# Performance work log

Measured on AMD Instinct MI355X. Metric: run time of the kernel, lower is better.

Reference implementation:

```python
import jax, jax.numpy as jnp
import numpy as np

# dims
B, S, H = 2, 256, 1024          # batch, global seq, global hidden
BH, NH = 384, 8                  # byte_hidden, num heads
HD = BH // NH                    # head dim = 48
P = 4                            # num_global_proj (seed byte positions)
S_C = 12                         # byte decode steps (= target.shape[2])
L = 4                            # num_byte_decoder_layers
V = 258                          # byte vocab (256 bytes + pad 256 + eos 257)
T = P + S_C
EOS = 257
SCALE = 1.0 / np.sqrt(HD)


def setup_inputs() -> dict:
    key = jax.random.key(0)
    ks = jax.random.split(key, 12)
    w = lambda k, shp: jax.random.normal(k, shp, jnp.float32) * 0.02
    return {
        "x": jax.random.normal(ks[0], (B, S, H), jnp.float32),
        "target": jax.random.randint(ks[1], (B, S, S_C), 0, V),
        "Wproj": w(ks[2], (H, P * BH)),
        "attn_norm": jnp.ones((L, BH), jnp.float32),
        "Wq": w(ks[3], (L, BH, BH)),
        "Wk": w(ks[4], (L, BH, BH)),
        "Wv": w(ks[5], (L, BH, BH)),
        "Wo": w(ks[6], (L, BH, BH)),
        "ffn_norm": jnp.ones((L, BH), jnp.float32),
        "W1": w(ks[7], (L, BH, 4 * BH)),
        "W2": w(ks[8], (L, 4 * BH, BH)),
        "Wlm": w(ks[9], (BH, V)),
    }


def _rms(x, g):
    return x * jax.lax.rsqrt(jnp.mean(x * x, -1, keepdims=True) + 1e-5) * g


def _block(x, kc, vc, pos, an, Wq, Wk, Wv, Wo, fn, W1, W2, causal):
    # x: [N, Lq, BH]; kc/vc: [N, T, NH, HD] KV caches; pos: static write offset
    N, Lq, _ = x.shape
    h = _rms(x, an)
    q = (h @ Wq).reshape(N, Lq, NH, HD)
    k = (h @ Wk).reshape(N, Lq, NH, HD)
    v = (h @ Wv).reshape(N, Lq, NH, HD)
    kc = jax.lax.dynamic_update_slice(kc, k, (0, pos, 0, 0))
    vc = jax.lax.dynamic_update_slice(vc, v, (0, pos, 0, 0))
    nk = pos + Lq
    sc = jnp.einsum('nqhd,nkhd->nhqk', q, kc[:, :nk]) * SCALE
    if causal:
        mask = jnp.arange(nk)[None, :] <= (pos + jnp.arange(Lq))[:, None]
        sc = jnp.where(mask[None, None], sc, jnp.float32(-1e30))
    p = jax.nn.softmax(sc, axis=-1)
    o = jnp.einsum('nhqk,nkhd->nqhd', p, vc[:, :nk]).reshape(N, Lq, BH)
    x = x + o @ Wo
    x = x + jax.nn.gelu(_rms(x, fn) @ W1, approximate=False) @ W2
    return x, kc, vc


def _forward(x, Wproj, attn_norm, Wq, Wk, Wv, Wo, ffn_norm, W1, W2, Wlm):
    N = B * S
    x0 = (x.reshape(N, H) @ Wproj).reshape(N, P, BH)
    x_out = jnp.zeros((N, T, BH), x0.dtype).at[:, :P].set(x0)
    kc = [jnp.zeros((N, T, NH, HD), x0.dtype) for _ in range(L)]
    vc = [jnp.zeros((N, T, NH, HD), x0.dtype) for _ in range(L)]
    finished = jnp.zeros((N,), bool)
    for i in range(S_C):
        if i == 0:
            pos, xi, causal = 0, x_out[:, :P], True          # prefill seed bytes
        else:
            pos, xi, causal = P + i - 1, x_out[:, P + i - 1:P + i], False  # decode 1 token
        for l in range(L):
            xi, kc[l], vc[l] = _block(xi, kc[l], vc[l], pos,
                                      attn_norm[l], Wq[l], Wk[l], Wv[l], Wo[l],
                                      ffn_norm[l], W1[l], W2[l], causal)
        gen = xi[:, -1]                                       # [N, BH]
        unf = ~finished
        # scatter only unfinished streams back (finished stay zero, as in torch)
        x_out = x_out.at[:, P + i].set(jnp.where(unf[:, None], gen, jnp.float32(0.0)))
        finished = finished | (unf & (jnp.argmax(gen, -1) == EOS))
    return x_out.reshape(B, S, T, BH)[:, :, P:, :] @ Wlm      # [B,S,S_C,V]


def reference(x, target, Wproj, attn_norm, Wq, Wk, Wv, Wo, ffn_norm, W1, W2, Wlm):
    del target  # only sets S_c (static here)
    return _forward(x, Wproj, attn_norm, Wq, Wk, Wv, Wo, ffn_norm, W1, W2, Wlm)
```

## Files before the change

kernel.cpp:

```cpp
#include <hip/hip_runtime.h>
#include <hip/hip_bf16.h>


constexpr int H_IN  = 1024;
constexpr int BH    = 384;
constexpr int NH    = 8;
constexpr int HD    = 48;
constexpr int PP    = 4;
constexpr int S_CNT = 12;
constexpr int NL    = 4;
constexpr int NV    = 258;
constexpr int TT    = 16;
constexpr int NSEQ  = 512;
constexpr int EOS_I = 257;
constexpr int NTH   = 768;
constexpr float RSCALE = 0.14433756729740646f;

typedef _Float16 h2 __attribute__((ext_vector_type(2)));
typedef _Float16 h8 __attribute__((ext_vector_type(8)));

union W16 { h8 v8; h2 h[4]; _Float16 e[8]; };

template<int N> struct IC { static constexpr int value = N; };

__device__ __forceinline__ float fdot2(h2 a, h2 b, float c) {
#if __has_builtin(__builtin_amdgcn_fdot2)
  return __builtin_amdgcn_fdot2(a, b, c, false);
#else
  return c + (float)a.x * (float)b.x + (float)a.y * (float)b.y;
#endif
}

__global__ __launch_bounds__(256)
void pack8_kernel(const float* __restrict__ src, const float* __restrict__ g,
                  h8* __restrict__ dst, int C) {
  int c  = blockIdx.x * 256 + threadIdx.x;
  int j8 = blockIdx.y;
  if (c < C) {
    h8 v;
    #pragma unroll
    for (int r = 0; r < 8; r++) {
      int row = 8 * j8 + r;
      float s = g ? g[row] : 1.0f;
      v[r] = (_Float16)(src[(size_t)row * C + c] * s);
    }
    dst[(size_t)j8 * C + c] = v;
  }
}

__global__ __launch_bounds__(NTH)
void decoder_kernel(const float* __restrict__ x,
                    const h8* __restrict__ Wproj8,
                    const h8* __restrict__ Wq8,
                    const h8* __restrict__ Wk8,
                    const h8* __restrict__ Wv8,
                    const h8* __restrict__ Wo8,
                    const h8* __restrict__ W18,
                    const h8* __restrict__ W28,
                    const h8* __restrict__ Wlm8,
                    float* __restrict__ out,
                    _Float16* __restrict__ kbuf,
                    _Float16* __restrict__ vbuf)
{
  __shared__ float xs[2][4][BH];
  __shared__ __align__(16) _Float16 xh[2][4][BH];
  __shared__ __align__(16) _Float16 qh[2][4][BH];
  __shared__ __align__(16) _Float16 oh[2][4][BH];
  __shared__ float sc[2][NH][4][TT];
  __shared__ __align__(16) union Scr {
    float qkvp[3][2][4][BH];
    float wop[2][4][BH];
    struct { __align__(16) _Float16 f1h[2][4][4*BH];
             float w2p[2][4][BH]; } ffn;
    __align__(16) _Float16 xin[2][H_IN];
  } scr;
  __shared__ float redsq[2][4][6];
  __shared__ float redv[12];
  __shared__ int   redi[12];
  __shared__ int   fin[2];

  const int tid = threadIdx.x;
  const int kg  = tid / BH;
  const int col = tid - kg * BH;
  const int sq  = kg;
  const int wid = tid >> 6;
  const int w6  = wid % 6;
  const int seq0 = blockIdx.x * 2;

  if (tid < 2) fin[tid] = 0;

  for (int s = 0; s < 2; s++) {
    const size_t base = (size_t)(seq0 + s) * H_IN;
    for (int j = tid; j < H_IN; j += NTH) scr.xin[s][j] = (_Float16)x[base + j];
  }
  __syncthreads();
  {
    float acc[2][2] = {};
    for (int j8 = 0; j8 < H_IN / 8; j8 += 4) {
      W16 w0[4], w1[4];
      #pragma unroll
      for (int u = 0; u < 4; u++) {
        w0[u].v8 = Wproj8[(size_t)(j8 + u) * (PP * BH) + tid];
        w1[u].v8 = Wproj8[(size_t)(j8 + u) * (PP * BH) + tid + NTH];
      }
      #pragma unroll
      for (int u = 0; u < 4; u++)
        #pragma unroll
        for (int s = 0; s < 2; s++) {
          W16 hv; hv.v8 = *(const h8*)&scr.xin[s][(j8 + u) * 8];
          #pragma unroll
          for (int r = 0; r < 4; r++) {
            acc[s][0] = fdot2(hv.h[r], w0[u].h[r], acc[s][0]);
            acc[s][1] = fdot2(hv.h[r], w1[u].h[r], acc[s][1]);
          }
        }
    }
    const int m0 = tid / BH, cc = tid - m0 * BH;
    #pragma unroll
    for (int s = 0; s < 2; s++) {
      xs[s][m0][cc]     = acc[s][0];  xh[s][m0][cc]     = (_Float16)acc[s][0];
      xs[s][m0 + 2][cc] = acc[s][1];  xh[s][m0 + 2][cc] = (_Float16)acc[s][1];
      float r0 = acc[s][0] * acc[s][0], r1 = acc[s][1] * acc[s][1];
      #pragma unroll
      for (int off = 32; off; off >>= 1) {
        r0 += __shfl_down(r0, off, 64); r1 += __shfl_down(r1, off, 64);
      }
      if ((tid & 63) == 0) { redsq[s][m0][w6] = r0; redsq[s][m0 + 2][w6] = r1; }
    }
  }
  __syncthreads();

  auto layers = [&](auto ntc, int pos, bool causal) {
    constexpr int NT = decltype(ntc)::value;
    const int nk = pos + NT;
    for (int l = 0; l < NL; l++) {
      {
        const size_t wb = ((size_t)l * 48 + kg * 24) * BH + col;
        float aq[2][NT] = {}, ak[2][NT] = {}, av[2][NT] = {};
        for (int j8 = 0; j8 < 24; j8 += 4) {
          W16 wq[4], wk[4], wv[4];
          #pragma unroll
          for (int u = 0; u < 4; u++) {
            wq[u].v8 = Wq8[wb + (size_t)(j8 + u) * BH];
            wk[u].v8 = Wk8[wb + (size_t)(j8 + u) * BH];
            wv[u].v8 = Wv8[wb + (size_t)(j8 + u) * BH];
          }
          #pragma unroll
          for (int u = 0; u < 4; u++)
            #pragma unroll
            for (int s = 0; s < 2; s++)
              #pragma unroll
              for (int tok = 0; tok < NT; tok++) {
                W16 hv; hv.v8 = *(const h8*)&xh[s][tok][(kg * 24 + j8 + u) * 8];
                #pragma unroll
                for (int r = 0; r < 4; r++) {
                  aq[s][tok] = fdot2(hv.h[r], wq[u].h[r], aq[s][tok]);
                  ak[s][tok] = fdot2(hv.h[r], wk[u].h[r], ak[s][tok]);
                  av[s][tok] = fdot2(hv.h[r], wv[u].h[r], av[s][tok]);
                }
              }
        }
        if (kg == 1) {
          #pragma unroll
          for (int s = 0; s < 2; s++)
            #pragma unroll
            for (int tok = 0; tok < NT; tok++) {
              scr.qkvp[0][s][tok][col] = aq[s][tok];
              scr.qkvp[1][s][tok][col] = ak[s][tok];
              scr.qkvp[2][s][tok][col] = av[s][tok];
            }
        }
        __syncthreads();
        if (kg == 0) {
          #pragma unroll
          for (int s = 0; s < 2; s++) {
            const size_t cb = (((size_t)(seq0 + s) * NL + l) * TT + pos) * BH + col;
            #pragma unroll
            for (int tok = 0; tok < NT; tok++) {
              float ss = redsq[s][tok][0] + redsq[s][tok][1] + redsq[s][tok][2] +
                         redsq[s][tok][3] + redsq[s][tok][4] + redsq[s][tok][5];
              float sca = rsqrtf(ss * (1.0f / BH) + 1e-5f);
              qh[s][tok][col] = (_Float16)((aq[s][tok] + scr.qkvp[0][s][tok][col]) * sca * RSCALE);
              kbuf[cb + (size_t)tok * BH] = (_Float16)((ak[s][tok] + scr.qkvp[1][s][tok][col]) * sca);
              vbuf[cb + (size_t)tok * BH] = (_Float16)((av[s][tok] + scr.qkvp[2][s][tok][col]) * sca);
            }
          }
        }
        __syncthreads();
      }
      {
        const int nu = 2 * NH * NT * nk;
        if (tid < nu) {
          int s = tid / (NH * NT * nk), r = tid % (NH * NT * nk);
          int h = r / (NT * nk); int r2 = r % (NT * nk);
          int qi = r2 / nk, j = r2 % nk;
          float d;
          if (causal && j > pos + qi) d = -1e30f;
          else {
            const h8* kp8 = (const h8*)(kbuf + (((size_t)(seq0 + s) * NL + l) * TT + j) * BH + h * HD);
            W16 kk[6];
            #pragma unroll
            for (int c = 0; c < 6; c++) kk[c].v8 = kp8[c];
            d = 0.f;
            #pragma unroll
            for (int c = 0; c < 6; c++)
              #pragma unroll
              for (int e = 0; e < 8; e++)
                d += (float)qh[s][qi][h * HD + c * 8 + e] * (float)kk[c].e[e];
          }
          sc[s][h][qi][j] = d;
        }
      }
      __syncthreads();
      {
        const int nr = 2 * NH * NT;
        if (tid < nr) {
          int s = tid / (NH * NT), r = tid % (NH * NT);
          int h = r / NT, qi = r % NT;
          float m = -3.0e38f;
          for (int j = 0; j < nk; j++) m = fmaxf(m, sc[s][h][qi][j]);
          float den = 0.f;
          for (int j = 0; j < nk; j++) {
            float e = expf(sc[s][h][qi][j] - m);
            sc[s][h][qi][j] = e; den += e;
          }
          float inv = 1.0f / den;
          for (int j = 0; j < nk; j++) sc[s][h][qi][j] *= inv;
        }
      }
      __syncthreads();
      {
        const size_t vb = (((size_t)(seq0 + sq) * NL + l) * TT) * BH + col;
        const int h = col / HD;
        #pragma unroll
        for (int tok = 0; tok < NT; tok++) {
          float acc = 0.f;
          int j = 0;
          for (; j + 4 <= nk; j += 4) {
            float v0 = (float)vbuf[vb + (size_t)(j + 0) * BH];
            float v1 = (float)vbuf[vb + (size_t)(j + 1) * BH];
            float v2 = (float)vbuf[vb + (size_t)(j + 2) * BH];
            float v3 = (float)vbuf[vb + (size_t)(j + 3) * BH];
            acc += sc[sq][h][tok][j] * v0 + sc[sq][h][tok][j+1] * v1 +
                   sc[sq][h][tok][j+2] * v2 + sc[sq][h][tok][j+3] * v3;
          }
          for (; j < nk; j++)
            acc += sc[sq][h][tok][j] * (float)vbuf[vb + (size_t)j * BH];
          oh[sq][tok][col] = (_Float16)acc;
        }
      }
      __syncthreads();
      {
        const size_t wb = ((size_t)l * 48 + kg * 24) * BH + col;
        float ao[2][NT] = {};
        for (int j8 = 0; j8 < 24; j8 += 8) {
          W16 w[8];
          #pragma unroll
          for (int u = 0; u < 8; u++) w[u].v8 = Wo8[wb + (size_t)(j8 + u) * BH];
          #pragma unroll
          for (int u = 0; u < 8; u++)
            #pragma unroll
            for (int s = 0; s < 2; s++)
              #pragma unroll
              for (int tok = 0; tok < NT; tok++) {
                W16 hv; hv.v8 = *(const h8*)&oh[s][tok][(kg * 24 + j8 + u) * 8];
                #pragma unroll
                for (int r = 0; r < 4; r++)
                  ao[s][tok] = fdot2(hv.h[r], w[u].h[r], ao[s][tok]);
              }
        }
        if (kg == 1) {
          #pragma unroll
          for (int s = 0; s < 2; s++)
            #pragma unroll
            for (int tok = 0; tok < NT; tok++) scr.wop[s][tok][col] = ao[s][tok];
        }
        __syncthreads();
        if (kg == 0) {
          #pragma unroll
          for (int s = 0; s < 2; s++)
            #pragma unroll
            for (int tok = 0; tok < NT; tok++) {
              float xn = xs[s][tok][col] + ao[s][tok] + scr.wop[s][tok][col];
              xs[s][tok][col] = xn; xh[s][tok][col] = (_Float16)xn;
              float r = xn * xn;
              #pragma unroll
              for (int off = 32; off; off >>= 1) r += __shfl_down(r, off, 64);
              if ((tid & 63) == 0) redsq[s][tok][wid] = r;
            }
        }
        __syncthreads();
      }
      {
        float a1[2][NT][2] = {};
        for (int j8 = 0; j8 < 48; j8 += 4) {
          W16 w0[4], w1[4];
          #pragma unroll
          for (int u = 0; u < 4; u++) {
            w0[u].v8 = W18[((size_t)(l * 48 + j8 + u)) * (4 * BH) + tid];
            w1[u].v8 = W18[((size_t)(l * 48 + j8 + u)) * (4 * BH) + tid + NTH];
          }
          #pragma unroll
          for (int u = 0; u < 4; u++)
            #pragma unroll
            for (int s = 0; s < 2; s++)
              #pragma unroll
              for (int t = 0; t < NT; t++) {
                W16 hv; hv.v8 = *(const h8*)&xh[s][t][(j8 + u) * 8];
                #pragma unroll
                for (int r = 0; r < 4; r++) {
                  a1[s][t][0] = fdot2(hv.h[r], w0[u].h[r], a1[s][t][0]);
                  a1[s][t][1] = fdot2(hv.h[r], w1[u].h[r], a1[s][t][1]);
                }
              }
        }
        #pragma unroll
        for (int s = 0; s < 2; s++)
          #pragma unroll
          for (int t = 0; t < NT; t++) {
            float ss = redsq[s][t][0] + redsq[s][t][1] + redsq[s][t][2] +
                       redsq[s][t][3] + redsq[s][t][4] + redsq[s][t][5];
            float sca = rsqrtf(ss * (1.0f / BH) + 1e-5f);
            float z0 = a1[s][t][0] * sca, z1 = a1[s][t][1] * sca;
            scr.ffn.f1h[s][t][tid]       = (_Float16)(0.5f * z0 * (1.0f + erff(z0 * 0.7071067811865476f)));
            scr.ffn.f1h[s][t][tid + NTH] = (_Float16)(0.5f * z1 * (1.0f + erff(z1 * 0.7071067811865476f)));
          }
        __syncthreads();
        {
          float a2[2][NT] = {};
          for (int j8 = 0; j8 < 96; j8 += 8) {
            W16 w[8];
            #pragma unroll
            for (int u = 0; u < 8; u++)
              w[u].v8 = W28[((size_t)(l * 192 + kg * 96 + j8 + u)) * BH + col];
            #pragma unroll
            for (int u = 0; u < 8; u++)
              #pragma unroll
              for (int s = 0; s < 2; s++)
                #pragma unroll
                for (int t = 0; t < NT; t++) {
                  W16 fv; fv.v8 = *(const h8*)&scr.ffn.f1h[s][t][(kg * 96 + j8 + u) * 8];
                  #pragma unroll
                  for (int r = 0; r < 4; r++)
                    a2[s][t] = fdot2(fv.h[r], w[u].h[r], a2[s][t]);
                }
          }
          if (kg == 1) {
            #pragma unroll
            for (int s = 0; s < 2; s++)
              #pragma unroll
              for (int t = 0; t < NT; t++) scr.ffn.w2p[s][t][col] = a2[s][t];
          }
          __syncthreads();
          if (kg == 0) {
            #pragma unroll
            for (int s = 0; s < 2; s++)
              #pragma unroll
              for (int t = 0; t < NT; t++) {
                float xn = xs[s][t][col] + a2[s][t] + scr.ffn.w2p[s][t][col];
                xs[s][t][col] = xn; xh[s][t][col] = (_Float16)xn;
                float r = xn * xn;
                #pragma unroll
                for (int off = 32; off; off >>= 1) r += __shfl_down(r, off, 64);
                if ((tid & 63) == 0) redsq[s][t][wid] = r;
              }
          }
          __syncthreads();
        }
      }
    }
  };

  for (int i = 0; i < S_CNT; i++) {
    int grow;
    if (i == 0) { layers(IC<4>{}, 0, true);           grow = 3; }
    else        { layers(IC<1>{}, PP + i - 1, false); grow = 0; }

    {
      float gen = xs[sq][grow][col];
      float v = gen; int idx = col;
      #pragma unroll
      for (int off = 32; off; off >>= 1) {
        float v2 = __shfl_down(v, off, 64); int i2 = __shfl_down(idx, off, 64);
        if (v2 > v || (v2 == v && i2 < idx)) { v = v2; idx = i2; }
      }
      if ((tid & 63) == 0) { redv[wid] = v; redi[wid] = idx; }
      float nxt = fin[sq] ? 0.0f : gen;
      xs[sq][0][col] = nxt; xh[sq][0][col] = (_Float16)nxt;
      float r = nxt * nxt;
      #pragma unroll
      for (int off = 32; off; off >>= 1) r += __shfl_down(r, off, 64);
      if ((tid & 63) == 0) redsq[sq][0][w6] = r;
      __syncthreads();
    }
    {
      if (col == 0) {
        const int b = sq * 6;
        float bv = redv[b]; int bi = redi[b];
        for (int w = 1; w < 6; w++)
          if (redv[b + w] > bv || (redv[b + w] == bv && redi[b + w] < bi)) {
            bv = redv[b + w]; bi = redi[b + w];
          }
        if (bi == EOS_I) fin[sq] = 1;
      }
      if (col < NV) {
        float acc = 0.f;
        for (int j8 = 0; j8 < 48; j8 += 8) {
          W16 w[8];
          #pragma unroll
          for (int u = 0; u < 8; u++) w[u].v8 = Wlm8[(size_t)(j8 + u) * NV + col];
          #pragma unroll
          for (int u = 0; u < 8; u++) {
            W16 gv; gv.v8 = *(const h8*)&xh[sq][0][(j8 + u) * 8];
            #pragma unroll
            for (int r = 0; r < 4; r++) acc = fdot2(gv.h[r], w[u].h[r], acc);
          }
        }
        out[((size_t)(seq0 + sq) * S_CNT + i) * NV + col] = acc;
      }
      __syncthreads();
    }
  }
}

extern "C" void kernel_launch(void* const* d_in, const int* in_sizes, int n_in,
                              void* d_out, int out_size, void* d_ws, size_t ws_size,
                              hipStream_t stream) {
  const float* x     = (const float*)d_in[0];
  const float* Wproj = (const float*)d_in[2];
  const float* an    = (const float*)d_in[3];
  const float* Wq    = (const float*)d_in[4];
  const float* Wk    = (const float*)d_in[5];
  const float* Wv    = (const float*)d_in[6];
  const float* Wo    = (const float*)d_in[7];
  const float* fn    = (const float*)d_in[8];
  const float* W1    = (const float*)d_in[9];
  const float* W2    = (const float*)d_in[10];
  const float* Wlm   = (const float*)d_in[11];
  float* out = (float*)d_out;
  (void)ws_size; (void)in_sizes; (void)n_in; (void)out_size;

  h8* w = (h8*)d_ws;
  const int n_proj = (H_IN / 8) * (PP * BH);
  const int n_qkvo = NL * (BH / 8) * BH;
  const int n_w1   = NL * (BH / 8) * (4 * BH);
  const int n_w2   = NL * (4 * BH / 8) * BH;
  const int n_lm   = (BH / 8) * NV;
  h8* Wproj_p = w;  w += n_proj;
  h8* Wq_p    = w;  w += n_qkvo;
  h8* Wk_p    = w;  w += n_qkvo;
  h8* Wv_p    = w;  w += n_qkvo;
  h8* Wo_p    = w;  w += n_qkvo;
  h8* W1_p    = w;  w += n_w1;
  h8* W2_p    = w;  w += n_w2;
  h8* Wlm_p   = w;  w += n_lm;
  const size_t kv_elems = (size_t)NSEQ * NL * TT * BH;
  _Float16* kbuf = (_Float16*)w;
  _Float16* vbuf = kbuf + kv_elems;

  auto pack = [&](const float* src, const float* g, h8* dst, int R, int C) {
    dim3 grid((C + 255) / 256, R / 8);
    pack8_kernel<<<grid, 256, 0, stream>>>(src, g, dst, C);
  };
  pack(Wproj, nullptr, Wproj_p, H_IN,        PP * BH);
  pack(Wq,    an,      Wq_p,    NL * BH,     BH);
  pack(Wk,    an,      Wk_p,    NL * BH,     BH);
  pack(Wv,    an,      Wv_p,    NL * BH,     BH);
  pack(Wo,    nullptr, Wo_p,    NL * BH,     BH);
  pack(W1,    fn,      W1_p,    NL * BH,     4 * BH);
  pack(W2,    nullptr, W2_p,    NL * 4 * BH, BH);
  pack(Wlm,   nullptr, Wlm_p,   BH,          NV);

  decoder_kernel<<<NSEQ / 2, NTH, 0, stream>>>(
      x, Wproj_p, Wq_p, Wk_p, Wv_p, Wo_p, W1_p, W2_p, Wlm_p, out, kbuf, vbuf);
}
```

Baseline: 2.422 ms.

## Double-buffer weight loads, split reduction epilogues, fuse decode attention softmax

```diff
diff --git a/kernel.cpp b/kernel.cpp
--- a/kernel.cpp
+++ b/kernel.cpp
@@ -47,6 +47,151 @@
     dst[(size_t)j8 * C + c] = v;
   }
 }
+
+#define QKV_DECL(S) W16 S##q0, S##q1, S##q2, S##q3, S##k0, S##k1, S##k2, S##k3, \
+                        S##v0, S##v1, S##v2, S##v3;
+#define QKV_LOAD(S, b) \
+  S##q0.v8 = Wq8[wb + (size_t)((b) + 0) * BH]; \
+  S##q1.v8 = Wq8[wb + (size_t)((b) + 1) * BH]; \
+  S##q2.v8 = Wq8[wb + (size_t)((b) + 2) * BH]; \
+  S##q3.v8 = Wq8[wb + (size_t)((b) + 3) * BH]; \
+  S##k0.v8 = Wk8[wb + (size_t)((b) + 0) * BH]; \
+  S##k1.v8 = Wk8[wb + (size_t)((b) + 1) * BH]; \
+  S##k2.v8 = Wk8[wb + (size_t)((b) + 2) * BH]; \
+  S##k3.v8 = Wk8[wb + (size_t)((b) + 3) * BH]; \
+  S##v0.v8 = Wv8[wb + (size_t)((b) + 0) * BH]; \
+  S##v1.v8 = Wv8[wb + (size_t)((b) + 1) * BH]; \
+  S##v2.v8 = Wv8[wb + (size_t)((b) + 2) * BH]; \
+  S##v3.v8 = Wv8[wb + (size_t)((b) + 3) * BH];
+#define QKV_COMP(S, b) \
+  _Pragma("unroll") \
+  for (int s_ = 0; s_ < 2; s_++) { \
+    _Pragma("unroll") \
+    for (int t_ = 0; t_ < NT; t_++) { \
+      W16 h0_, h1_, h2_, h3_; \
+      h0_.v8 = *(const h8*)&xh[s_][t_][(kg * 24 + (b) + 0) * 8]; \
+      h1_.v8 = *(const h8*)&xh[s_][t_][(kg * 24 + (b) + 1) * 8]; \
+      h2_.v8 = *(const h8*)&xh[s_][t_][(kg * 24 + (b) + 2) * 8]; \
+      h3_.v8 = *(const h8*)&xh[s_][t_][(kg * 24 + (b) + 3) * 8]; \
+      _Pragma("unroll") \
+      for (int r_ = 0; r_ < 4; r_++) { \
+        aq[s_][t_] = fdot2(h0_.h[r_], S##q0.h[r_], aq[s_][t_]); \
+        ak[s_][t_] = fdot2(h0_.h[r_], S##k0.h[r_], ak[s_][t_]); \
+        av[s_][t_] = fdot2(h0_.h[r_], S##v0.h[r_], av[s_][t_]); \
+        aq[s_][t_] = fdot2(h1_.h[r_], S##q1.h[r_], aq[s_][t_]); \
+        ak[s_][t_] = fdot2(h1_.h[r_], S##k1.h[r_], ak[s_][t_]); \
+        av[s_][t_] = fdot2(h1_.h[r_], S##v1.h[r_], av[s_][t_]); \
+        aq[s_][t_] = fdot2(h2_.h[r_], S##q2.h[r_], aq[s_][t_]); \
+        ak[s_][t_] = fdot2(h2_.h[r_], S##k2.h[r_], ak[s_][t_]); \
+        av[s_][t_] = fdot2(h2_.h[r_], S##v2.h[r_], av[s_][t_]); \
+        aq[s_][t_] = fdot2(h3_.h[r_], S##q3.h[r_], aq[s_][t_]); \
+        ak[s_][t_] = fdot2(h3_.h[r_], S##k3.h[r_], ak[s_][t_]); \
+        av[s_][t_] = fdot2(h3_.h[r_], S##v3.h[r_], av[s_][t_]); \
+      } } }
+
+#define WO_DECL(S) W16 S##o0, S##o1, S##o2, S##o3, S##o4, S##o5, S##o6, S##o7;
+#define WO_LOAD(S, b) \
+  S##o0.v8 = Wo8[wb + (size_t)((b) + 0) * BH]; \
+  S##o1.v8 = Wo8[wb + (size_t)((b) + 1) * BH]; \
+  S##o2.v8 = Wo8[wb + (size_t)((b) + 2) * BH]; \
+  S##o3.v8 = Wo8[wb + (size_t)((b) + 3) * BH]; \
+  S##o4.v8 = Wo8[wb + (size_t)((b) + 4) * BH]; \
+  S##o5.v8 = Wo8[wb + (size_t)((b) + 5) * BH]; \
+  S##o6.v8 = Wo8[wb + (size_t)((b) + 6) * BH]; \
+  S##o7.v8 = Wo8[wb + (size_t)((b) + 7) * BH];
+#define WO_COMP(S, b) \
+  _Pragma("unroll") \
+  for (int s_ = 0; s_ < 2; s_++) { \
+    _Pragma("unroll") \
+    for (int t_ = 0; t_ < NT; t_++) { \
+      W16 h0_, h1_, h2_, h3_, h4_, h5_, h6_, h7_; \
+      h0_.v8 = *(const h8*)&oh[s_][t_][(kg * 24 + (b) + 0) * 8]; \
+      h1_.v8 = *(const h8*)&oh[s_][t_][(kg * 24 + (b) + 1) * 8]; \
+      h2_.v8 = *(const h8*)&oh[s_][t_][(kg * 24 + (b) + 2) * 8]; \
+      h3_.v8 = *(const h8*)&oh[s_][t_][(kg * 24 + (b) + 3) * 8]; \
+      h4_.v8 = *(const h8*)&oh[s_][t_][(kg * 24 + (b) + 4) * 8]; \
+      h5_.v8 = *(const h8*)&oh[s_][t_][(kg * 24 + (b) + 5) * 8]; \
+      h6_.v8 = *(const h8*)&oh[s_][t_][(kg * 24 + (b) + 6) * 8]; \
+      h7_.v8 = *(const h8*)&oh[s_][t_][(kg * 24 + (b) + 7) * 8]; \
+      _Pragma("unroll") \
+      for (int r_ = 0; r_ < 4; r_++) { \
+        ao[s_][t_] = fdot2(h0_.h[r_], S##o0.h[r_], ao[s_][t_]); \
+        ao[s_][t_] = fdot2(h1_.h[r_], S##o1.h[r_], ao[s_][t_]); \
+        ao[s_][t_] = fdot2(h2_.h[r_], S##o2.h[r_], ao[s_][t_]); \
+        ao[s_][t_] = fdot2(h3_.h[r_], S##o3.h[r_], ao[s_][t_]); \
+        ao[s_][t_] = fdot2(h4_.h[r_], S##o4.h[r_], ao[s_][t_]); \
+        ao[s_][t_] = fdot2(h5_.h[r_], S##o5.h[r_], ao[s_][t_]); \
+        ao[s_][t_] = fdot2(h6_.h[r_], S##o6.h[r_], ao[s_][t_]); \
+        ao[s_][t_] = fdot2(h7_.h[r_], S##o7.h[r_], ao[s_][t_]); \
+      } } }
+
+#define W1_DECL(S) W16 S##a0, S##a1, S##a2, S##a3, S##b0, S##b1, S##b2, S##b3;
+#define W1_LOAD(S, b) \
+  S##a0.v8 = W18[((size_t)(l * 48 + (b) + 0)) * (4 * BH) + tid]; \
+  S##a1.v8 = W18[((size_t)(l * 48 + (b) + 1)) * (4 * BH) + tid]; \
+  S##a2.v8 = W18[((size_t)(l * 48 + (b) + 2)) * (4 * BH) + tid]; \
+  S##a3.v8 = W18[((size_t)(l * 48 + (b) + 3)) * (4 * BH) + tid]; \
+  S##b0.v8 = W18[((size_t)(l * 48 + (b) + 0)) * (4 * BH) + tid + NTH]; \
+  S##b1.v8 = W18[((size_t)(l * 48 + (b) + 1)) * (4 * BH) + tid + NTH]; \
+  S##b2.v8 = W18[((size_t)(l * 48 + (b) + 2)) * (4 * BH) + tid + NTH]; \
+  S##b3.v8 = W18[((size_t)(l * 48 + (b) + 3)) * (4 * BH) + tid + NTH];
+#define W1_COMP(S, b) \
+  _Pragma("unroll") \
+  for (int s_ = 0; s_ < 2; s_++) { \
+    _Pragma("unroll") \
+    for (int t_ = 0; t_ < NT; t_++) { \
+      W16 h0_, h1_, h2_, h3_; \
+      h0_.v8 = *(const h8*)&xh[s_][t_][((b) + 0) * 8]; \
+      h1_.v8 = *(const h8*)&xh[s_][t_][((b) + 1) * 8]; \
+      h2_.v8 = *(const h8*)&xh[s_][t_][((b) + 2) * 8]; \
+      h3_.v8 = *(const h8*)&xh[s_][t_][((b) + 3) * 8]; \
+      _Pragma("unroll") \
+      for (int r_ = 0; r_ < 4; r_++) { \
+        a1[s_][t_][0] = fdot2(h0_.h[r_], S##a0.h[r_], a1[s_][t_][0]); \
+        a1[s_][t_][1] = fdot2(h0_.h[r_], S##b0.h[r_], a1[s_][t_][1]); \
+        a1[s_][t_][0] = fdot2(h1_.h[r_], S##a1.h[r_], a1[s_][t_][0]); \
+        a1[s_][t_][1] = fdot2(h1_.h[r_], S##b1.h[r_], a1[s_][t_][1]); \
+        a1[s_][t_][0] = fdot2(h2_.h[r_], S##a2.h[r_], a1[s_][t_][0]); \
+        a1[s_][t_][1] = fdot2(h2_.h[r_], S##b2.h[r_], a1[s_][t_][1]); \
+        a1[s_][t_][0] = fdot2(h3_.h[r_], S##a3.h[r_], a1[s_][t_][0]); \
+        a1[s_][t_][1] = fdot2(h3_.h[r_], S##b3.h[r_], a1[s_][t_][1]); \
+      } } }
+
+#define W2_DECL(S) W16 S##g0, S##g1, S##g2, S##g3, S##g4, S##g5, S##g6, S##g7;
+#define W2_LOAD(S, b) \
+  S##g0.v8 = W28[((size_t)(l * 192 + kg * 96 + (b) + 0)) * BH + col]; \
+  S##g1.v8 = W28[((size_t)(l * 192 + kg * 96 + (b) + 1)) * BH + col]; \
+  S##g2.v8 = W28[((size_t)(l * 192 + kg * 96 + (b) + 2)) * BH + col]; \
+  S##g3.v8 = W28[((size_t)(l * 192 + kg * 96 + (b) + 3)) * BH + col]; \
+  S##g4.v8 = W28[((size_t)(l * 192 + kg * 96 + (b) + 4)) * BH + col]; \
+  S##g5.v8 = W28[((size_t)(l * 192 + kg * 96 + (b) + 5)) * BH + col]; \
+  S##g6.v8 = W28[((size_t)(l * 192 + kg * 96 + (b) + 6)) * BH + col]; \
+  S##g7.v8 = W28[((size_t)(l * 192 + kg * 96 + (b) + 7)) * BH + col];
+#define W2_COMP(S, b) \
+  _Pragma("unroll") \
+  for (int s_ = 0; s_ < 2; s_++) { \
+    _Pragma("unroll") \
+    for (int t_ = 0; t_ < NT; t_++) { \
+      W16 f0_, f1_, f2_, f3_, f4_, f5_, f6_, f7_; \
+      f0_.v8 = *(const h8*)&scr.ffn.f1h[s_][t_][(kg * 96 + (b) + 0) * 8]; \
+      f1_.v8 = *(const h8*)&scr.ffn.f1h[s_][t_][(kg * 96 + (b) + 1) * 8]; \
+      f2_.v8 = *(const h8*)&scr.ffn.f1h[s_][t_][(kg * 96 + (b) + 2) * 8]; \
+      f3_.v8 = *(const h8*)&scr.ffn.f1h[s_][t_][(kg * 96 + (b) + 3) * 8]; \
+      f4_.v8 = *(const h8*)&scr.ffn.f1h[s_][t_][(kg * 96 + (b) + 4) * 8]; \
+      f5_.v8 = *(const h8*)&scr.ffn.f1h[s_][t_][(kg * 96 + (b) + 5) * 8]; \
+      f6_.v8 = *(const h8*)&scr.ffn.f1h[s_][t_][(kg * 96 + (b) + 6) * 8]; \
+      f7_.v8 = *(const h8*)&scr.ffn.f1h[s_][t_][(kg * 96 + (b) + 7) * 8]; \
+      _Pragma("unroll") \
+      for (int r_ = 0; r_ < 4; r_++) { \
+        a2[s_][t_] = fdot2(f0_.h[r_], S##g0.h[r_], a2[s_][t_]); \
+        a2[s_][t_] = fdot2(f1_.h[r_], S##g1.h[r_], a2[s_][t_]); \
+        a2[s_][t_] = fdot2(f2_.h[r_], S##g2.h[r_], a2[s_][t_]); \
+        a2[s_][t_] = fdot2(f3_.h[r_], S##g3.h[r_], a2[s_][t_]); \
+        a2[s_][t_] = fdot2(f4_.h[r_], S##g4.h[r_], a2[s_][t_]); \
+        a2[s_][t_] = fdot2(f5_.h[r_], S##g5.h[r_], a2[s_][t_]); \
+        a2[s_][t_] = fdot2(f6_.h[r_], S##g6.h[r_], a2[s_][t_]); \
+        a2[s_][t_] = fdot2(f7_.h[r_], S##g7.h[r_], a2[s_][t_]); \
+      } } }
 
 __global__ __launch_bounds__(NTH)
 void decoder_kernel(const float* __restrict__ x,
@@ -137,98 +282,113 @@
       {
         const size_t wb = ((size_t)l * 48 + kg * 24) * BH + col;
         float aq[2][NT] = {}, ak[2][NT] = {}, av[2][NT] = {};
-        for (int j8 = 0; j8 < 24; j8 += 4) {
-          W16 wq[4], wk[4], wv[4];
-          #pragma unroll
-          for (int u = 0; u < 4; u++) {
-            wq[u].v8 = Wq8[wb + (size_t)(j8 + u) * BH];
-            wk[u].v8 = Wk8[wb + (size_t)(j8 + u) * BH];
-            wv[u].v8 = Wv8[wb + (size_t)(j8 + u) * BH];
-          }
-          #pragma unroll
-          for (int u = 0; u < 4; u++)
-            #pragma unroll
-            for (int s = 0; s < 2; s++)
-              #pragma unroll
-              for (int tok = 0; tok < NT; tok++) {
-                W16 hv; hv.v8 = *(const h8*)&xh[s][tok][(kg * 24 + j8 + u) * 8];
-                #pragma unroll
-                for (int r = 0; r < 4; r++) {
-                  aq[s][tok] = fdot2(hv.h[r], wq[u].h[r], aq[s][tok]);
-                  ak[s][tok] = fdot2(hv.h[r], wk[u].h[r], ak[s][tok]);
-                  av[s][tok] = fdot2(hv.h[r], wv[u].h[r], av[s][tok]);
-                }
-              }
-        }
-        if (kg == 1) {
-          #pragma unroll
-          for (int s = 0; s < 2; s++)
-            #pragma unroll
-            for (int tok = 0; tok < NT; tok++) {
-              scr.qkvp[0][s][tok][col] = aq[s][tok];
-              scr.qkvp[1][s][tok][col] = ak[s][tok];
-              scr.qkvp[2][s][tok][col] = av[s][tok];
-            }
-        }
-        __syncthreads();
-        if (kg == 0) {
-          #pragma unroll
-          for (int s = 0; s < 2; s++) {
-            const size_t cb = (((size_t)(seq0 + s) * NL + l) * TT + pos) * BH + col;
-            #pragma unroll
-            for (int tok = 0; tok < NT; tok++) {
-              float ss = redsq[s][tok][0] + redsq[s][tok][1] + redsq[s][tok][2] +
-                         redsq[s][tok][3] + redsq[s][tok][4] + redsq[s][tok][5];
-              float sca = rsqrtf(ss * (1.0f / BH) + 1e-5f);
-              qh[s][tok][col] = (_Float16)((aq[s][tok] + scr.qkvp[0][s][tok][col]) * sca * RSCALE);
-              kbuf[cb + (size_t)tok * BH] = (_Float16)((ak[s][tok] + scr.qkvp[1][s][tok][col]) * sca);
-              vbuf[cb + (size_t)tok * BH] = (_Float16)((av[s][tok] + scr.qkvp[2][s][tok][col]) * sca);
-            }
-          }
-        }
-        __syncthreads();
-      }
-      {
-        const int nu = 2 * NH * NT * nk;
-        if (tid < nu) {
-          int s = tid / (NH * NT * nk), r = tid % (NH * NT * nk);
-          int h = r / (NT * nk); int r2 = r % (NT * nk);
-          int qi = r2 / nk, j = r2 % nk;
-          float d;
-          if (causal && j > pos + qi) d = -1e30f;
-          else {
+        QKV_DECL(A) QKV_DECL(B)
+        QKV_LOAD(A, 0)
+        QKV_LOAD(B, 4)
+        QKV_COMP(A, 0)
+        QKV_LOAD(A, 8)
+        QKV_COMP(B, 4)
+        QKV_LOAD(B, 12)
+        QKV_COMP(A, 8)
+        QKV_LOAD(A, 16)
+        QKV_COMP(B, 12)
+        QKV_LOAD(B, 20)
+        QKV_COMP(A, 16)
+        QKV_COMP(B, 20)
+        {
+          const int so = kg ^ 1;
+          #pragma unroll
+          for (int tok = 0; tok < NT; tok++) {
+            scr.qkvp[0][so][tok][col] = aq[so][tok];
+            scr.qkvp[1][so][tok][col] = ak[so][tok];
+            scr.qkvp[2][so][tok][col] = av[so][tok];
+          }
+        }
+        __syncthreads();
+        {
+          const int s = kg;
+          const size_t cb = (((size_t)(seq0 + s) * NL + l) * TT + pos) * BH + col;
+          #pragma unroll
+          for (int tok = 0; tok < NT; tok++) {
+            float ss = redsq[s][tok][0] + redsq[s][tok][1] + redsq[s][tok][2] +
+                       redsq[s][tok][3] + redsq[s][tok][4] + redsq[s][tok][5];
+            float sca = rsqrtf(ss * (1.0f / BH) + 1e-5f);
+            qh[s][tok][col] = (_Float16)((aq[s][tok] + scr.qkvp[0][s][tok][col]) * sca * RSCALE);
+            kbuf[cb + (size_t)tok * BH] = (_Float16)((ak[s][tok] + scr.qkvp[1][s][tok][col]) * sca);
+            vbuf[cb + (size_t)tok * BH] = (_Float16)((av[s][tok] + scr.qkvp[2][s][tok][col]) * sca);
+          }
+        }
+        __syncthreads();
+      }
+      if constexpr (NT == 1) {
+        if (tid < 2 * NH * TT) {
+          const int s = tid >> 7, r = tid & 127, h = r >> 4, j = r & 15;
+          float d = -1e30f;
+          if (j < nk) {
             const h8* kp8 = (const h8*)(kbuf + (((size_t)(seq0 + s) * NL + l) * TT + j) * BH + h * HD);
-            W16 kk[6];
-            #pragma unroll
-            for (int c = 0; c < 6; c++) kk[c].v8 = kp8[c];
             d = 0.f;
             #pragma unroll
-            for (int c = 0; c < 6; c++)
+            for (int c6 = 0; c6 < 6; c6++) {
+              W16 kk, qq;
+              kk.v8 = kp8[c6];
+              qq.v8 = *(const h8*)&qh[s][0][h * HD + c6 * 8];
               #pragma unroll
-              for (int e = 0; e < 8; e++)
-                d += (float)qh[s][qi][h * HD + c * 8 + e] * (float)kk[c].e[e];
-          }
-          sc[s][h][qi][j] = d;
-        }
-      }
-      __syncthreads();
-      {
-        const int nr = 2 * NH * NT;
-        if (tid < nr) {
-          int s = tid / (NH * NT), r = tid % (NH * NT);
-          int h = r / NT, qi = r % NT;
-          float m = -3.0e38f;
-          for (int j = 0; j < nk; j++) m = fmaxf(m, sc[s][h][qi][j]);
-          float den = 0.f;
-          for (int j = 0; j < nk; j++) {
-            float e = expf(sc[s][h][qi][j] - m);
-            sc[s][h][qi][j] = e; den += e;
-          }
-          float inv = 1.0f / den;
-          for (int j = 0; j < nk; j++) sc[s][h][qi][j] *= inv;
-        }
-      }
-      __syncthreads();
+              for (int rr = 0; rr < 4; rr++) d = fdot2(qq.h[rr], kk.h[rr], d);
+            }
+          }
+          float m = d;
+          #pragma unroll
+          for (int off = 8; off; off >>= 1) m = fmaxf(m, __shfl_xor(m, off, 16));
+          float e = expf(d - m);
+          float den = e;
+          #pragma unroll
+          for (int off = 8; off; off >>= 1) den += __shfl_xor(den, off, 16);
+          sc[s][h][0][j] = e * (1.0f / den);
+        }
+        __syncthreads();
+      } else {
+        {
+          const int nu = 2 * NH * NT * nk;
+          if (tid < nu) {
+            int s = tid / (NH * NT * nk), r = tid % (NH * NT * nk);
+            int h = r / (NT * nk); int r2 = r % (NT * nk);
+            int qi = r2 / nk, j = r2 % nk;
+            float d;
+            if (causal && j > pos + qi) d = -1e30f;
+            else {
+              const h8* kp8 = (const h8*)(kbuf + (((size_t)(seq0 + s) * NL + l) * TT + j) * BH + h * HD);
+              d = 0.f;
+              #pragma unroll
+              for (int c6 = 0; c6 < 6; c6++) {
+                W16 kk, qq;
+                kk.v8 = kp8[c6];
+                qq.v8 = *(const h8*)&qh[s][qi][h * HD + c6 * 8];
+                #pragma unroll
+                for (int rr = 0; rr < 4; rr++) d = fdot2(qq.h[rr], kk.h[rr], d);
+              }
+            }
+            sc[s][h][qi][j] = d;
+          }
+        }
+        __syncthreads();
+        {
+          const int nr = 2 * NH * NT;
+          if (tid < nr) {
+            int s = tid / (NH * NT), r = tid % (NH * NT);
+            int h = r / NT, qi = r % NT;
+            float m = -3.0e38f;
+            for (int j = 0; j < nk; j++) m = fmaxf(m, sc[s][h][qi][j]);
+            float den = 0.f;
+            for (int j = 0; j < nk; j++) {
+              float e = expf(sc[s][h][qi][j] - m);
+              sc[s][h][qi][j] = e; den += e;
+            }
+            float inv = 1.0f / den;
+            for (int j = 0; j < nk; j++) sc[s][h][qi][j] *= inv;
+          }
+        }
+        __syncthreads();
+      }
       {
         const size_t vb = (((size_t)(seq0 + sq) * NL + l) * TT) * BH + col;
         const int h = col / HD;
@@ -241,8 +401,8 @@
             float v1 = (float)vbuf[vb + (size_t)(j + 1) * BH];
             float v2 = (float)vbuf[vb + (size_t)(j + 2) * BH];
             float v3 = (float)vbuf[vb + (size_t)(j + 3) * BH];
-            acc += sc[sq][h][tok][j] * v0 + sc[sq][h][tok][j+1] * v1 +
-                   sc[sq][h][tok][j+2] * v2 + sc[sq][h][tok][j+3] * v3;
+            acc += sc[sq][h][tok][j] * v0 + sc[sq][h][tok][j + 1] * v1 +
+                   sc[sq][h][tok][j + 2] * v2 + sc[sq][h][tok][j + 3] * v3;
           }
           for (; j < nk; j++)
             acc += sc[sq][h][tok][j] * (float)vbuf[vb + (size_t)j * BH];
@@ -253,66 +413,61 @@
       {
         const size_t wb = ((size_t)l * 48 + kg * 24) * BH + col;
         float ao[2][NT] = {};
-        for (int j8 = 0; j8 < 24; j8 += 8) {
-          W16 w[8];
-          #pragma unroll
-          for (int u = 0; u < 8; u++) w[u].v8 = Wo8[wb + (size_t)(j8 + u) * BH];
-          #pragma unroll
-          for (int u = 0; u < 8; u++)
+        WO_DECL(A) WO_DECL(B)
+        WO_LOAD(A, 0)
+        WO_LOAD(B, 8)
+        WO_COMP(A, 0)
+        WO_LOAD(A, 16)
+        WO_COMP(B, 8)
+        WO_COMP(A, 16)
+        {
+          const int so = kg ^ 1;
+          #pragma unroll
+          for (int tok = 0; tok < NT; tok++) scr.wop[so][tok][col] = ao[so][tok];
+        }
+        __syncthreads();
+        {
+          const int s = kg;
+          #pragma unroll
+          for (int tok = 0; tok < NT; tok++) {
+            float xn = xs[s][tok][col] + ao[s][tok] + scr.wop[s][tok][col];
+            xs[s][tok][col] = xn; xh[s][tok][col] = (_Float16)xn;
+            float r = xn * xn;
             #pragma unroll
-            for (int s = 0; s < 2; s++)
-              #pragma unroll
-              for (int tok = 0; tok < NT; tok++) {
-                W16 hv; hv.v8 = *(const h8*)&oh[s][tok][(kg * 24 + j8 + u) * 8];
-                #pragma unroll
-                for (int r = 0; r < 4; r++)
-                  ao[s][tok] = fdot2(hv.h[r], w[u].h[r], ao[s][tok]);
-              }
-        }
-        if (kg == 1) {
-          #pragma unroll
-          for (int s = 0; s < 2; s++)
-            #pragma unroll
-            for (int tok = 0; tok < NT; tok++) scr.wop[s][tok][col] = ao[s][tok];
-        }
-        __syncthreads();
-        if (kg == 0) {
-          #pragma unroll
-          for (int s = 0; s < 2; s++)
-            #pragma unroll
-            for (int tok = 0; tok < NT; tok++) {
-              float xn = xs[s][tok][col] + ao[s][tok] + scr.wop[s][tok][col];
-              xs[s][tok][col] = xn; xh[s][tok][col] = (_Float16)xn;
-              float r = xn * xn;
-              #pragma unroll
-              for (int off = 32; off; off >>= 1) r += __shfl_down(r, off, 64);
-              if ((tid & 63) == 0) redsq[s][tok][wid] = r;
-            }
+            for (int off = 32; off; off >>= 1) r += __shfl_down(r, off, 64);
+            if ((tid & 63) == 0) redsq[s][tok][w6] = r;
+          }
         }
         __syncthreads();
       }
       {
         float a1[2][NT][2] = {};
-        for (int j8 = 0; j8 < 48; j8 += 4) {
-          W16 w0[4], w1[4];
-          #pragma unroll
-          for (int u = 0; u < 4; u++) {
-            w0[u].v8 = W18[((size_t)(l * 48 + j8 + u)) * (4 * BH) + tid];
-            w1[u].v8 = W18[((size_t)(l * 48 + j8 + u)) * (4 * BH) + tid + NTH];
-          }
-          #pragma unroll
-          for (int u = 0; u < 4; u++)
-            #pragma unroll
-            for (int s = 0; s < 2; s++)
-              #pragma unroll
-              for (int t = 0; t < NT; t++) {
-                W16 hv; hv.v8 = *(const h8*)&xh[s][t][(j8 + u) * 8];
-                #pragma unroll
-                for (int r = 0; r < 4; r++) {
-                  a1[s][t][0] = fdot2(hv.h[r], w0[u].h[r], a1[s][t][0]);
-                  a1[s][t][1] = fdot2(hv.h[r], w1[u].h[r], a1[s][t][1]);
-                }
-              }
+        {
+          W1_DECL(A) W1_DECL(B)
+          W1_LOAD(A, 0)
+          W1_LOAD(B, 4)
+          W1_COMP(A, 0)
+          W1_LOAD(A, 8)
+          W1_COMP(B, 4)
+          W1_LOAD(B, 12)
+          W1_COMP(A, 8)
+          W1_LOAD(A, 16)
+          W1_COMP(B, 12)
+          W1_LOAD(B, 20)
+          W1_COMP(A, 16)
+          W1_LOAD(A, 24)
+          W1_COMP(B, 20)
+          W1_LOAD(B, 28)
+          W1_COMP(A, 24)
+          W1_LOAD(A, 32)
+          W1_COMP(B, 28)
+          W1_LOAD(B, 36)
+          W1_COMP(A, 32)
+          W1_LOAD(A, 40)
+          W1_COMP(B, 36)
+          W1_LOAD(B, 44)
+          W1_COMP(A, 40)
+          W1_COMP(B, 44)
         }
         #pragma unroll
         for (int s = 0; s < 2; s++)
@@ -328,42 +483,48 @@
         __syncthreads();
         {
           float a2[2][NT] = {};
-          for (int j8 = 0; j8 < 96; j8 += 8) {
-            W16 w[8];
+          W2_DECL(A) W2_DECL(B)
+          W2_LOAD(A, 0)
+          W2_LOAD(B, 8)
+          W2_COMP(A, 0)
+          W2_LOAD(A, 16)
+          W2_COMP(B, 8)
+          W2_LOAD(B, 24)
+          W2_COMP(A, 16)
+          W2_LOAD(A, 32)
+          W2_COMP(B, 24)
+          W2_LOAD(B, 40)
+          W2_COMP(A, 32)
+          W2_LOAD(A, 48)
+          W2_COMP(B, 40)
+          W2_LOAD(B, 56)
+          W2_COMP(A, 48)
+          W2_LOAD(A, 64)
+          W2_COMP(B, 56)
+          W2_LOAD(B, 72)
+          W2_COMP(A, 64)
+          W2_LOAD(A, 80)
+          W2_COMP(B, 72)
+          W2_LOAD(B, 88)
+          W2_COMP(A, 80)
+          W2_COMP(B, 88)
+          {
+            const int so = kg ^ 1;
             #pragma unroll
-            for (int u = 0; u < 8; u++)
-              w[u].v8 = W28[((size_t)(l * 192 + kg * 96 + j8 + u)) * BH + col];
+            for (int t = 0; t < NT; t++) scr.ffn.w2p[so][t][col] = a2[so][t];
+          }
+          __syncthreads();
+          {
+            const int s = kg;
             #pragma unroll
-            for (int u = 0; u < 8; u++)
+            for (int t = 0; t < NT; t++) {
+              float xn = xs[s][t][col] + a2[s][t] + scr.ffn.w2p[s][t][col];
+              xs[s][t][col] = xn; xh[s][t][col] = (_Float16)xn;
+              float r = xn * xn;
               #pragma unroll
-              for (int s = 0; s < 2; s++)
-                #pragma unroll
-                for (int t = 0; t < NT; t++) {
-                  W16 fv; fv.v8 = *(const h8*)&scr.ffn.f1h[s][t][(kg * 96 + j8 + u) * 8];
-                  #pragma unroll
-                  for (int r = 0; r < 4; r++)
-                    a2[s][t] = fdot2(fv.h[r], w[u].h[r], a2[s][t]);
-                }
-          }
-          if (kg == 1) {
-            #pragma unroll
-            for (int s = 0; s < 2; s++)
-              #pragma unroll
-              for (int t = 0; t < NT; t++) scr.ffn.w2p[s][t][col] = a2[s][t];
-          }
-          __syncthreads();
-          if (kg == 0) {
-            #pragma unroll
-            for (int s = 0; s < 2; s++)
-              #pragma unroll
-              for (int t = 0; t < NT; t++) {
-                float xn = xs[s][t][col] + a2[s][t] + scr.ffn.w2p[s][t][col];
-                xs[s][t][col] = xn; xh[s][t][col] = (_Float16)xn;
-                float r = xn * xn;
-                #pragma unroll
-                for (int off = 32; off; off >>= 1) r += __shfl_down(r, off, 64);
-                if ((tid & 63) == 0) redsq[s][t][wid] = r;
-              }
+              for (int off = 32; off; off >>= 1) r += __shfl_down(r, off, 64);
+              if ((tid & 63) == 0) redsq[s][t][w6] = r;
+            }
           }
           __syncthreads();
         }
```

After: 7.625 ms. 3.15x slower.

## Split-K reduction across both thread groups, fuse decode softmax via shuffles

Applied to the files above, without the earlier changes.

```diff
diff --git a/kernel.cpp b/kernel.cpp
--- a/kernel.cpp
+++ b/kernel.cpp
@@ -66,6 +66,8 @@
   __shared__ __align__(16) _Float16 xh[2][4][BH];
   __shared__ __align__(16) _Float16 qh[2][4][BH];
   __shared__ __align__(16) _Float16 oh[2][4][BH];
+  __shared__ __align__(16) _Float16 k_cur[2][4][BH];
+  __shared__ __align__(16) _Float16 v_cur[2][4][BH];
   __shared__ float sc[2][NH][4][TT];
   __shared__ __align__(16) union Scr {
     float qkvp[3][2][4][BH];
@@ -160,92 +162,129 @@
                 }
               }
         }
-        if (kg == 1) {
-          #pragma unroll
-          for (int s = 0; s < 2; s++)
-            #pragma unroll
-            for (int tok = 0; tok < NT; tok++) {
-              scr.qkvp[0][s][tok][col] = aq[s][tok];
-              scr.qkvp[1][s][tok][col] = ak[s][tok];
-              scr.qkvp[2][s][tok][col] = av[s][tok];
+        {
+          const int so = kg ^ 1;
+          #pragma unroll
+          for (int tok = 0; tok < NT; tok++) {
+            scr.qkvp[0][so][tok][col] = aq[so][tok];
+            scr.qkvp[1][so][tok][col] = ak[so][tok];
+            scr.qkvp[2][so][tok][col] = av[so][tok];
+          }
+        }
+        __syncthreads();
+        {
+          const int s = kg;
+          const size_t cb = (((size_t)(seq0 + s) * NL + l) * TT + pos) * BH + col;
+          #pragma unroll
+          for (int tok = 0; tok < NT; tok++) {
+            float ss = redsq[s][tok][0] + redsq[s][tok][1] + redsq[s][tok][2] +
+                       redsq[s][tok][3] + redsq[s][tok][4] + redsq[s][tok][5];
+            float sca = rsqrtf(ss * (1.0f / BH) + 1e-5f);
+            float kv_ = (ak[s][tok] + scr.qkvp[1][s][tok][col]) * sca;
+            float vv_ = (av[s][tok] + scr.qkvp[2][s][tok][col]) * sca;
+            qh[s][tok][col] = (_Float16)((aq[s][tok] + scr.qkvp[0][s][tok][col]) * sca * RSCALE);
+            k_cur[s][tok][col] = (_Float16)kv_;
+            v_cur[s][tok][col] = (_Float16)vv_;
+            kbuf[cb + (size_t)tok * BH] = (_Float16)kv_;
+            vbuf[cb + (size_t)tok * BH] = (_Float16)vv_;
+          }
+        }
+        __syncthreads();
+      }
+      if constexpr (NT == 1) {
+        if (tid < 2 * NH * TT) {
+          const int s = tid >> 7, r = tid & 127, h = r >> 4, j = r & 15;
+          float d = -1e30f;
+          if (j < nk) {
+            const h8* kp8 = (j == pos)
+                ? (const h8*)&k_cur[s][0][h * HD]
+                : (const h8*)(kbuf + (((size_t)(seq0 + s) * NL + l) * TT + j) * BH + h * HD);
+            d = 0.f;
+            #pragma unroll
+            for (int c6 = 0; c6 < 6; c6++) {
+              W16 kk, qq;
+              kk.v8 = kp8[c6];
+              qq.v8 = *(const h8*)&qh[s][0][h * HD + c6 * 8];
+              #pragma unroll
+              for (int rr = 0; rr < 4; rr++) d = fdot2(qq.h[rr], kk.h[rr], d);
             }
-        }
-        __syncthreads();
-        if (kg == 0) {
-          #pragma unroll
-          for (int s = 0; s < 2; s++) {
-            const size_t cb = (((size_t)(seq0 + s) * NL + l) * TT + pos) * BH + col;
-            #pragma unroll
-            for (int tok = 0; tok < NT; tok++) {
-              float ss = redsq[s][tok][0] + redsq[s][tok][1] + redsq[s][tok][2] +
-                         redsq[s][tok][3] + redsq[s][tok][4] + redsq[s][tok][5];
-              float sca = rsqrtf(ss * (1.0f / BH) + 1e-5f);
-              qh[s][tok][col] = (_Float16)((aq[s][tok] + scr.qkvp[0][s][tok][col]) * sca * RSCALE);
-              kbuf[cb + (size_t)tok * BH] = (_Float16)((ak[s][tok] + scr.qkvp[1][s][tok][col]) * sca);
-              vbuf[cb + (size_t)tok * BH] = (_Float16)((av[s][tok] + scr.qkvp[2][s][tok][col]) * sca);
+          }
+          float m = d;
+          #pragma unroll
+          for (int off = 8; off; off >>= 1) m = fmaxf(m, __shfl_xor(m, off, 16));
+          float e = expf(d - m);
+          float den = e;
+          #pragma unroll
+          for (int off = 8; off; off >>= 1) den += __shfl_xor(den, off, 16);
+          sc[s][h][0][j] = e * (1.0f / den);
+        }
+        __syncthreads();
+      } else {
+        {
+          const int nu = 2 * NH * NT * nk;
+          if (tid < nu) {
+            int s = tid / (NH * NT * nk), r = tid % (NH * NT * nk);
+            int h = r / (NT * nk); int r2 = r % (NT * nk);
+            int qi = r2 / nk, j = r2 % nk;
+            float d;
+            if (causal && j > pos + qi) d = -1e30f;
+            else {
+              d = 0.f;
+              #pragma unroll
+              for (int c6 = 0; c6 < 6; c6++) {
+                W16 kk, qq;
+                kk.v8 = *(const h8*)&k_cur[s][j][h * HD + c6 * 8];
+                qq.v8 = *(const h8*)&qh[s][qi][h * HD + c6 * 8];
+                #pragma unroll
+                for (int rr = 0; rr < 4; rr++) d = fdot2(qq.h[rr], kk.h[rr], d);
+              }
             }
-          }
-        }
-        __syncthreads();
-      }
-      {
-        const int nu = 2 * NH * NT * nk;
-        if (tid < nu) {
-          int s = tid / (NH * NT * nk), r = tid % (NH * NT * nk);
-          int h = r / (NT * nk); int r2 = r % (NT * nk);
-          int qi = r2 / nk, j = r2 % nk;
-          float d;
-          if (causal && j > pos + qi) d = -1e30f;
-          else {
-            const h8* kp8 = (const h8*)(kbuf + (((size_t)(seq0 + s) * NL + l) * TT + j) * BH + h * HD);
-            W16 kk[6];
-            #pragma unroll
-            for (int c = 0; c < 6; c++) kk[c].v8 = kp8[c];
-            d = 0.f;
-            #pragma unroll
-            for (int c = 0; c < 6; c++)
-              #pragma unroll
-              for (int e = 0; e < 8; e++)
-                d += (float)qh[s][qi][h * HD + c * 8 + e] * (float)kk[c].e[e];
-          }
-          sc[s][h][qi][j] = d;
-        }
-      }
-      __syncthreads();
-      {
-        const int nr = 2 * NH * NT;
-        if (tid < nr) {
-          int s = tid / (NH * NT), r = tid % (NH * NT);
-          int h = r / NT, qi = r % NT;
-          float m = -3.0e38f;
-          for (int j = 0; j < nk; j++) m = fmaxf(m, sc[s][h][qi][j]);
-          float den = 0.f;
-          for (int j = 0; j < nk; j++) {
-            float e = expf(sc[s][h][qi][j] - m);
-            sc[s][h][qi][j] = e; den += e;
-          }
-          float inv = 1.0f / den;
-          for (int j = 0; j < nk; j++) sc[s][h][qi][j] *= inv;
-        }
-      }
-      __syncthreads();
+            sc[s][h][qi][j] = d;
+          }
+        }
+        __syncthreads();
+        {
+          const int nr = 2 * NH * NT;
+          if (tid < nr) {
+            int s = tid / (NH * NT), r = tid % (NH * NT);
+            int h = r / NT, qi = r % NT;
+            float m = -3.0e38f;
+            for (int j = 0; j < nk; j++) m = fmaxf(m, sc[s][h][qi][j]);
+            float den = 0.f;
+            for (int j = 0; j < nk; j++) {
+              float e = expf(sc[s][h][qi][j] - m);
+              sc[s][h][qi][j] = e; den += e;
+            }
+            float inv = 1.0f / den;
+            for (int j = 0; j < nk; j++) sc[s][h][qi][j] *= inv;
+          }
+        }
+        __syncthreads();
+      }
       {
         const size_t vb = (((size_t)(seq0 + sq) * NL + l) * TT) * BH + col;
         const int h = col / HD;
         #pragma unroll
         for (int tok = 0; tok < NT; tok++) {
           float acc = 0.f;
-          int j = 0;
-          for (; j + 4 <= nk; j += 4) {
-            float v0 = (float)vbuf[vb + (size_t)(j + 0) * BH];
-            float v1 = (float)vbuf[vb + (size_t)(j + 1) * BH];
-            float v2 = (float)vbuf[vb + (size_t)(j + 2) * BH];
-            float v3 = (float)vbuf[vb + (size_t)(j + 3) * BH];
-            acc += sc[sq][h][tok][j] * v0 + sc[sq][h][tok][j+1] * v1 +
-                   sc[sq][h][tok][j+2] * v2 + sc[sq][h][tok][j+3] * v3;
-          }
-          for (; j < nk; j++)
-            acc += sc[sq][h][tok][j] * (float)vbuf[vb + (size_t)j * BH];
+          if constexpr (NT == 1) {
+            int j = 0;
+            for (; j + 4 <= pos; j += 4) {
+              float v0 = (float)vbuf[vb + (size_t)(j + 0) * BH];
+              float v1 = (float)vbuf[vb + (size_t)(j + 1) * BH];
+              float v2 = (float)vbuf[vb + (size_t)(j + 2) * BH];
+              float v3 = (float)vbuf[vb + (size_t)(j + 3) * BH];
+              acc += sc[sq][h][0][j] * v0 + sc[sq][h][0][j + 1] * v1 +
+                     sc[sq][h][0][j + 2] * v2 + sc[sq][h][0][j + 3] * v3;
+            }
+            for (; j < pos; j++)
+              acc += sc[sq][h][0][j] * (float)vbuf[vb + (size_t)j * BH];
+            acc += sc[sq][h][0][pos] * (float)v_cur[sq][0][col];
+          } else {
+            #pragma unroll
+            for (int j = 0; j < 4; j++)
+              acc += sc[sq][h][tok][j] * (float)v_cur[sq][j][col];
+          }
           oh[sq][tok][col] = (_Float16)acc;
         }
       }
@@ -269,25 +308,23 @@
                   ao[s][tok] = fdot2(hv.h[r], w[u].h[r], ao[s][tok]);
               }
         }
-        if (kg == 1) {
-          #pragma unroll
-          for (int s = 0; s < 2; s++)
-            #pragma unroll
-            for (int tok = 0; tok < NT; tok++) scr.wop[s][tok][col] = ao[s][tok];
-        }
-        __syncthreads();
-        if (kg == 0) {
-          #pragma unroll
-          for (int s = 0; s < 2; s++)
-            #pragma unroll
-            for (int tok = 0; tok < NT; tok++) {
-              float xn = xs[s][tok][col] + ao[s][tok] + scr.wop[s][tok][col];
-              xs[s][tok][col] = xn; xh[s][tok][col] = (_Float16)xn;
-              float r = xn * xn;
-              #pragma unroll
-              for (int off = 32; off; off >>= 1) r += __shfl_down(r, off, 64);
-              if ((tid & 63) == 0) redsq[s][tok][wid] = r;
-            }
+        {
+          const int so = kg ^ 1;
+          #pragma unroll
+          for (int tok = 0; tok < NT; tok++) scr.wop[so][tok][col] = ao[so][tok];
+        }
+        __syncthreads();
+        {
+          const int s = kg;
+          #pragma unroll
+          for (int tok = 0; tok < NT; tok++) {
+            float xn = xs[s][tok][col] + ao[s][tok] + scr.wop[s][tok][col];
+            xs[s][tok][col] = xn; xh[s][tok][col] = (_Float16)xn;
+            float r = xn * xn;
+            #pragma unroll
+            for (int off = 32; off; off >>= 1) r += __shfl_down(r, off, 64);
+            if ((tid & 63) == 0) redsq[s][tok][w6] = r;
+          }
         }
         __syncthreads();
       }
@@ -345,25 +382,23 @@
                     a2[s][t] = fdot2(fv.h[r], w[u].h[r], a2[s][t]);
                 }
           }
-          if (kg == 1) {
-            #pragma unroll
-            for (int s = 0; s < 2; s++)
-              #pragma unroll
-              for (int t = 0; t < NT; t++) scr.ffn.w2p[s][t][col] = a2[s][t];
+          {
+            const int so = kg ^ 1;
+            #pragma unroll
+            for (int t = 0; t < NT; t++) scr.ffn.w2p[so][t][col] = a2[so][t];
           }
           __syncthreads();
-          if (kg == 0) {
-            #pragma unroll
-            for (int s = 0; s < 2; s++)
-              #pragma unroll
-              for (int t = 0; t < NT; t++) {
-                float xn = xs[s][t][col] + a2[s][t] + scr.ffn.w2p[s][t][col];
-                xs[s][t][col] = xn; xh[s][t][col] = (_Float16)xn;
-                float r = xn * xn;
-                #pragma unroll
-                for (int off = 32; off; off >>= 1) r += __shfl_down(r, off, 64);
-                if ((tid & 63) == 0) redsq[s][t][wid] = r;
-              }
+          {
+            const int s = kg;
+            #pragma unroll
+            for (int t = 0; t < NT; t++) {
+              float xn = xs[s][t][col] + a2[s][t] + scr.ffn.w2p[s][t][col];
+              xs[s][t][col] = xn; xh[s][t][col] = (_Float16)xn;
+              float r = xn * xn;
+              #pragma unroll
+              for (int off = 32; off; off >>= 1) r += __shfl_down(r, off, 64);
+              if ((tid & 63) == 0) redsq[s][t][w6] = r;
+            }
           }
           __syncthreads();
         }
```

Result: faster. 2.334 ms (-3.7%).
